# Performance work log

Measured on AMD Instinct MI355X. Metric: run time of the kernel, lower is better.

## Reference

```python
import jax, jax.numpy as jnp
import numpy as np

B, T, C, NH = 2, 2048, 1024, 16
HD = C // NH  # 64


def _ln(x, g, b, eps=1e-5):
    m = x.mean(-1, keepdims=True)
    v = ((x - m) ** 2).mean(-1, keepdims=True)
    return (x - m) / jnp.sqrt(v + eps) * g + b


def _ff(x, w1, b1, w2, b2):
    # Linear -> exact (erf) GELU -> Linear; dropout=0 (identity)
    return jax.nn.gelu(x @ w1 + b1, approximate=False) @ w2 + b2


def setup_inputs() -> dict:
    key = jax.random.key(0)
    ks = jax.random.split(key, 16)
    s = 0.02
    f32 = jnp.float32
    return {
        "x": jax.random.normal(ks[0], (B, T, C), f32),
        # SelfAttn qkv projection (torch Linear stored transposed: (in, out))
        "w_attn": jax.random.normal(ks[1], (C, 3 * C), f32) * s,
        "b_attn": jnp.zeros((3 * C,), f32),
        # SelfAttn's internal FeedForward
        "wa1": jax.random.normal(ks[2], (C, 4 * C), f32) * s,
        "ba1": jnp.zeros((4 * C,), f32),
        "wa2": jax.random.normal(ks[3], (4 * C, C), f32) * s,
        "ba2": jnp.zeros((C,), f32),
        # Block ln1
        "g1": jnp.ones((C,), f32),
        "be1": jnp.zeros((C,), f32),
        # Block FeedForward
        "wf1": jax.random.normal(ks[4], (C, 4 * C), f32) * s,
        "bf1": jnp.zeros((4 * C,), f32),
        "wf2": jax.random.normal(ks[5], (4 * C, C), f32) * s,
        "bf2": jnp.zeros((C,), f32),
        # Block ln2
        "g2": jnp.ones((C,), f32),
        "be2": jnp.zeros((C,), f32),
    }


def reference(x, w_attn, b_attn, wa1, ba1, wa2, ba2, g1, be1,
              wf1, bf1, wf2, bf2, g2, be2):
    Bx, Tx, Cx = x.shape
    qkv = x @ w_attn + b_attn  # (B, T, 3C)
    # NOTE: original splits as K, Q, V (in that order)
    K, Q, V = jnp.split(qkv, 3, axis=-1)

    def heads(t):  # (B, T, C) -> (B, NH, T, HD)
        return t.reshape(Bx, Tx, NH, HD).transpose(0, 2, 1, 3)

    Q, K, V = heads(Q), heads(K), heads(V)
    att = jnp.einsum('bhqd,bhkd->bhqk', Q, K) / np.float32(np.sqrt(HD))
    mask = jnp.tril(jnp.ones((Tx, Tx), bool))  # causal
    att = jnp.where(mask, att, -jnp.inf)
    att = jax.nn.softmax(att, axis=-1)
    y = jnp.einsum('bhqk,bhkd->bhqd', att, V)
    y = y.transpose(0, 2, 1, 3).reshape(Bx, Tx, Cx)
    # SelfAttn applies its own FeedForward (no output projection)
    y = _ff(y, wa1, ba1, wa2, ba2)
    # Block: post-sublayer LayerNorm, additive residuals
    x = x + _ln(y, g1, be1)
    x = x + _ln(_ff(x, wf1, bf1, wf2, bf2), g2, be2)
    return x
```

## Files before the change

kernel.cpp:

```cpp
#include <hip/hip_runtime.h>
#include <hip/hip_bf16.h>
#include <math.h>

#define Bz 2
#define Tz 2048
#define Cz 1024
#define NHz 16
#define HDz 64
#define Mz (Bz*Tz)

typedef unsigned short u16;
typedef __attribute__((ext_vector_type(8))) short bf16x8;
typedef __attribute__((ext_vector_type(4))) float f32x4;

__device__ __forceinline__ float bf2f(u16 u){
  union { unsigned int i; float f; } v; v.i = ((unsigned int)u) << 16; return v.f;
}
__device__ __forceinline__ u16 f2bf(float f){
  union { float f; unsigned int i; } v; v.f = f;
  return (u16)((v.i + 0x7fffu + ((v.i >> 16) & 1u)) >> 16);
}
__device__ __forceinline__ unsigned pack_bf_trunc(float a, float b){
  union { float f; unsigned u; } ua, ub; ua.f = a; ub.f = b;
  return (ua.u >> 16) | (ub.u & 0xffff0000u);
}
__device__ __forceinline__ float gelu_fast(float x){
  float x3 = x * x * x;
  float z2 = 1.5957691216057308f * (x + 0.044715f * x3);
  float e  = __expf(z2);
  float t  = 1.f - 2.f / (e + 1.f);
  return 0.5f * x * (1.f + t);
}

__device__ __forceinline__ void glds16(const void* g, void* l){
  __builtin_amdgcn_global_load_lds(
      (const __attribute__((address_space(1))) void*)g,
      (__attribute__((address_space(3))) void*)l, 16, 0, 0);
}

__global__ __launch_bounds__(256) void cast4_kernel(const float* __restrict__ in,
                                                    u16* __restrict__ out, int n4){
  int i = blockIdx.x * 256 + threadIdx.x;
  if (i < n4) {
    float4 v = ((const float4*)in)[i];
    u16 t[4] = { f2bf(v.x), f2bf(v.y), f2bf(v.z), f2bf(v.w) };
    *(uint2*)&out[(size_t)i * 4] = *(const uint2*)t;
  }
}

__global__ __launch_bounds__(256) void transpose5_kernel(
    const float* __restrict__ s0, const float* __restrict__ s1,
    const float* __restrict__ s2, const float* __restrict__ s3,
    const float* __restrict__ s4,
    u16* __restrict__ d0, u16* __restrict__ d1, u16* __restrict__ d2,
    u16* __restrict__ d3, u16* __restrict__ d4){
  __shared__ float tile[32][33];
  const int t = blockIdx.x;
  const float* src; u16* dst; int K, N, local;
  if (t < 3072)       { src = s0; dst = d0; K = 1024; N = 3072; local = t; }
  else if (t < 7168)  { src = s1; dst = d1; K = 1024; N = 4096; local = t - 3072; }
  else if (t < 11264) { src = s2; dst = d2; K = 4096; N = 1024; local = t - 7168; }
  else if (t < 15360) { src = s3; dst = d3; K = 1024; N = 4096; local = t - 11264; }
  else                { src = s4; dst = d4; K = 4096; N = 1024; local = t - 15360; }
  const int NT = N >> 5;
  const int kb = (local / NT) * 32, nb = (local % NT) * 32;
  const int tx = threadIdx.x & 31, ty = threadIdx.x >> 5;
  #pragma unroll
  for (int r = ty; r < 32; r += 8)
    tile[r][tx] = src[(size_t)(kb + r) * N + nb + tx];
  __syncthreads();
  #pragma unroll
  for (int r = ty; r < 32; r += 8)
    dst[(size_t)(nb + r) * K + kb + tx] = f2bf(tile[tx][r]);
}

template<int ACT>
__global__ __launch_bounds__(256) void gemm_kernel(const u16* __restrict__ A,
                                                   const u16* __restrict__ Bt,
                                                   const float* __restrict__ bias,
                                                   float* __restrict__ outf,
                                                   float* __restrict__ outf2,
                                                   u16* __restrict__ outb,
                                                   int N, int lda, int klen){
  __shared__ __align__(16) u16 As[2][128 * 32];
  __shared__ __align__(16) u16 Bs[2][128 * 32];
  const int tid  = threadIdx.x;
  const int wave = tid >> 6, lane = tid & 63;
  const int wm = (wave & 1) * 64, wn = (wave >> 1) * 64;
  const int m0 = blockIdx.x * 128, n0 = blockIdx.y * 128;
  const int kz = blockIdx.z;
  const int cc = lane & 15, quad = lane >> 4;
  const int lko = quad * 8;

  const u16* Ak  = A  + (size_t)kz * klen;
  const u16* Btk = Bt + (size_t)kz * klen;

  const int c = tid, c2 = tid + 256;
  const int row1 = c >> 2,  kc1 = (c & 3) * 8;
  const int row2 = c2 >> 2, kc2 = (c2 & 3) * 8;

  f32x4 acc[4][4] = {};

  const int nk = klen / 32;
  {
    glds16(Ak  + (size_t)(m0 + row1) * lda + kc1, &As[0][row1 * 32 + kc1]);
    glds16(Btk + (size_t)(n0 + row1) * lda + kc1, &Bs[0][row1 * 32 + kc1]);
    glds16(Ak  + (size_t)(m0 + row2) * lda + kc2, &As[0][row2 * 32 + kc2]);
    glds16(Btk + (size_t)(n0 + row2) * lda + kc2, &Bs[0][row2 * 32 + kc2]);
  }
  for (int ki = 0; ki < nk; ki++) {
    __syncthreads();
    if (ki + 1 < nk) {
      const int k0 = (ki + 1) * 32, bsel = (ki + 1) & 1;
      glds16(Ak  + (size_t)(m0 + row1) * lda + k0 + kc1, &As[bsel][row1 * 32 + kc1]);
      glds16(Btk + (size_t)(n0 + row1) * lda + k0 + kc1, &Bs[bsel][row1 * 32 + kc1]);
      glds16(Ak  + (size_t)(m0 + row2) * lda + k0 + kc2, &As[bsel][row2 * 32 + kc2]);
      glds16(Btk + (size_t)(n0 + row2) * lda + k0 + kc2, &Bs[bsel][row2 * 32 + kc2]);
    }
    const u16* Asb = As[ki & 1];
    const u16* Bsb = Bs[ki & 1];

    bf16x8 af[4], bfr[4];
    #pragma unroll
    for (int i = 0; i < 4; i++)
      af[i]  = *(const bf16x8*)&Asb[(wm + i * 16 + cc) * 32 + lko];
    #pragma unroll
    for (int j = 0; j < 4; j++)
      bfr[j] = *(const bf16x8*)&Bsb[(wn + j * 16 + cc) * 32 + lko];
    #pragma unroll
    for (int i = 0; i < 4; i++)
      #pragma unroll
      for (int j = 0; j < 4; j++)
        acc[i][j] = __builtin_amdgcn_mfma_f32_16x16x32_bf16(af[i], bfr[j], acc[i][j], 0, 0, 0);
  }

  const float* bias_k = (kz == 0) ? bias : nullptr;
  float* po = (kz == 0) ? outf : outf2;
  const int rbase = quad * 4;
  #pragma unroll
  for (int i = 0; i < 4; i++) {
    #pragma unroll
    for (int j = 0; j < 4; j++) {
      int col = n0 + wn + j * 16 + cc;
      float bv = bias_k ? bias_k[col] : 0.f;
      #pragma unroll
      for (int r = 0; r < 4; r++) {
        int row = m0 + wm + i * 16 + rbase + r;
        float v = acc[i][j][r] + bv;
        if (ACT == 1) v = gelu_fast(v);
        if (po)   po[(size_t)row * N + col]   = v;
        if (outb) outb[(size_t)row * N + col] = f2bf(v);
      }
    }
  }
}

__global__ __launch_bounds__(256) void vtrans_kernel(const u16* __restrict__ qkv,
                                                     u16* __restrict__ Vtb){
  __shared__ u16 Vl[64 * 72];
  const int tid = threadIdx.x;
  const int t0 = blockIdx.x * 64, h = blockIdx.y, b = blockIdx.z;
  const int bh = b * NHz + h;
  #pragma unroll
  for (int it = 0; it < 2; it++) {
    int c = tid + it * 256;
    int row = c >> 3, g = c & 7;
    *(uint4*)&Vl[row * 72 + g * 8] =
        *(const uint4*)(qkv + (size_t)(b * Tz + t0 + row) * (3 * Cz) + 2 * Cz + h * 64 + g * 8);
  }
  __syncthreads();
  #pragma unroll
  for (int it = 0; it < 2; it++) {
    int c = tid + it * 256;
    int d = c >> 3, tg = c & 7;
    u16 tmp[8];
    #pragma unroll
    for (int e = 0; e < 8; e++) tmp[e] = Vl[(tg * 8 + e) * 72 + d];
    *(uint4*)&Vtb[((size_t)bh * 64 + d) * Tz + t0 + tg * 8] = *(const uint4*)tmp;
  }
}

__global__ __launch_bounds__(256) void attn_kernel(const u16* __restrict__ qkv,
                                                   const u16* __restrict__ Vtb,
                                                   u16* __restrict__ y){
  __shared__ __align__(16) u16 KV[2][2][64 * 64];
  __shared__ __align__(16) u16 Ps[64 * 72];
  const int tid = threadIdx.x;
  const int lane = tid & 63, wave = tid >> 6;
  const int cc = lane & 15, quad = lane >> 4;
  const int h = blockIdx.y, b = blockIdx.z;
  const int bh = b * NHz + h;
  const size_t rowb = (size_t)b * Tz;
  const int wq0 = wave * 16;

  int foff[4][2];
  const int sw0 = (quad ^ (cc & 7)) * 8;
  const int sw1 = ((4 + quad) ^ (cc & 7)) * 8;
  #pragma unroll
  for (int t = 0; t < 4; ++t) {
    foff[t][0] = (t * 16 + cc) * 64 + sw0;
    foff[t][1] = (t * 16 + cc) * 64 + sw1;
  }
  const int pswb = (wq0 + cc) * 72 + quad * 4;
  const int psr0 = (wq0 + cc) * 72 + quad * 8;
  const int psr1 = (wq0 + cc) * 72 + 32 + quad * 8;

  auto stage = [&](int i, int bsel) {
    const int k0s = i * 64;
    #pragma unroll
    for (int it = 0; it < 2; ++it) {
      int ci = tid + it * 256;
      int row = ci >> 3, g = ci & 7;
      int gs = g ^ (row & 7);
      glds16(qkv + (rowb + k0s + row) * (3 * Cz) + h * 64 + gs * 8, &KV[bsel][0][ci * 8]);
      glds16(Vtb + ((size_t)bh * 64 + row) * Tz + k0s + gs * 8,     &KV[bsel][1][ci * 8]);
    }
  };

  for (int ph = 0; ph < 2; ++ph) {
    const int qt = ph ? (31 - (int)blockIdx.x) : (int)blockIdx.x;
    const int q0t = qt * 64 + wq0;
    const int nkt = qt + 1;
    const int wqmax = q0t + 15;

    bf16x8 qf[2];
    #pragma unroll
    for (int s = 0; s < 2; ++s)
      qf[s] = *(const bf16x8*)(qkv + (rowb + q0t + cc) * (3 * Cz)
                               + Cz + h * 64 + s * 32 + quad * 8);
    f32x4 acc[4] = {};
    float lp = 0.f;

    if (ph) __syncthreads();
    stage(0, 0);

    for (int i = 0; i < nkt; ++i) {
      __syncthreads();
      if (i + 1 < nkt) stage(i + 1, (i + 1) & 1);
      const int sel = i & 1;
      const u16* Kl = KV[sel][0];
      const u16* Vl = KV[sel][1];
      const int k0 = i * 64;
      if (k0 > wqmax) continue;

      bf16x8 kf[4][2];
      #pragma unroll
      for (int kt = 0; kt < 4; ++kt) {
        kf[kt][0] = *(const bf16x8*)&Kl[foff[kt][0]];
        kf[kt][1] = *(const bf16x8*)&Kl[foff[kt][1]];
      }
      const int qbase = q0t;
      #pragma unroll
      for (int kt = 0; kt < 4; ++kt) {
        const int kbase = k0 + kt * 16;
        uint2 pk;
        if (kbase > qbase + 15) {
          pk.x = 0u; pk.y = 0u;
        } else {
          f32x4 st = __builtin_amdgcn_mfma_f32_16x16x32_bf16(
              kf[kt][0], qf[0], (f32x4){0.f, 0.f, 0.f, 0.f}, 0, 0, 0);
          st = __builtin_amdgcn_mfma_f32_16x16x32_bf16(kf[kt][1], qf[1], st, 0, 0, 0);
          if (kbase + 15 > qbase) {
            const int kq = kbase + quad * 4, ql = qbase + cc;
            st[0] = (kq     <= ql) ? st[0] : -1e30f;
            st[1] = (kq + 1 <= ql) ? st[1] : -1e30f;
            st[2] = (kq + 2 <= ql) ? st[2] : -1e30f;
            st[3] = (kq + 3 <= ql) ? st[3] : -1e30f;
          }
          float p0 = __expf(fmaf(st[0], 0.125f, -16.f));
          float p1 = __expf(fmaf(st[1], 0.125f, -16.f));
          float p2 = __expf(fmaf(st[2], 0.125f, -16.f));
          float p3 = __expf(fmaf(st[3], 0.125f, -16.f));
          lp += (p0 + p1) + (p2 + p3);
          pk.x = pack_bf_trunc(p0, p1);
          pk.y = pack_bf_trunc(p2, p3);
        }
        *(uint2*)&Ps[pswb + kt * 16] = pk;
      }
      bf16x8 pf0 = *(const bf16x8*)&Ps[psr0];
      bf16x8 pf1 = *(const bf16x8*)&Ps[psr1];
      #pragma unroll
      for (int jd = 0; jd < 4; ++jd) {
        bf16x8 vf0 = *(const bf16x8*)&Vl[foff[jd][0]];
        bf16x8 vf1 = *(const bf16x8*)&Vl[foff[jd][1]];
        acc[jd] = __builtin_amdgcn_mfma_f32_16x16x32_bf16(pf0, vf0, acc[jd], 0, 0, 0);
        acc[jd] = __builtin_amdgcn_mfma_f32_16x16x32_bf16(pf1, vf1, acc[jd], 0, 0, 0);
      }
    }

    lp += __shfl_xor(lp, 16, 64);
    lp += __shfl_xor(lp, 32, 64);
    float inv[4];
    #pragma unroll
    for (int r = 0; r < 4; ++r) inv[r] = 1.f / __shfl(lp, quad * 4 + r, 64);
    #pragma unroll
    for (int jd = 0; jd < 4; ++jd)
      #pragma unroll
      for (int r = 0; r < 4; ++r) {
        int qrow = q0t + quad * 4 + r;
        y[(rowb + qrow) * Cz + h * 64 + jd * 16 + cc] = f2bf(acc[jd][r] * inv[r]);
      }
  }
}

__global__ __launch_bounds__(256) void ln_resid_kernel(const float* __restrict__ x,
                                                       const float* __restrict__ yin,
                                                       const float* __restrict__ yin2,
                                                       const float* __restrict__ g,
                                                       const float* __restrict__ be,
                                                       float* __restrict__ outf,
                                                       u16* __restrict__ outb){
  const int row = blockIdx.x;
  const int c0 = threadIdx.x * 4;
  const float* yr = yin + (size_t)row * Cz;
  const float* xr = x   + (size_t)row * Cz;
  float4 v = *(const float4*)(yr + c0);
  if (yin2) {
    float4 v2 = *(const float4*)(yin2 + (size_t)row * Cz + c0);
    v.x += v2.x; v.y += v2.y; v.z += v2.z; v.w += v2.w;
  }
  float s  = v.x + v.y + v.z + v.w;
  float s2 = v.x*v.x + v.y*v.y + v.z*v.z + v.w*v.w;
  #pragma unroll
  for (int off = 32; off > 0; off >>= 1) {
    s  += __shfl_down(s,  off);
    s2 += __shfl_down(s2, off);
  }
  __shared__ float ps[4], ps2[4];
  int wave = threadIdx.x >> 6, lane = threadIdx.x & 63;
  if (lane == 0) { ps[wave] = s; ps2[wave] = s2; }
  __syncthreads();
  s  = ps[0]  + ps[1]  + ps[2]  + ps[3];
  s2 = ps2[0] + ps2[1] + ps2[2] + ps2[3];
  const float mean = s * (1.f / Cz);
  const float var  = s2 * (1.f / Cz) - mean * mean;
  const float rstd = rsqrtf(var + 1e-5f);
  float4 xv = *(const float4*)(xr + c0);
  float4 gv = *(const float4*)(g + c0);
  float4 bv = *(const float4*)(be + c0);
  float4 ov;
  ov.x = xv.x + (v.x - mean) * rstd * gv.x + bv.x;
  ov.y = xv.y + (v.y - mean) * rstd * gv.y + bv.y;
  ov.z = xv.z + (v.z - mean) * rstd * gv.z + bv.z;
  ov.w = xv.w + (v.w - mean) * rstd * gv.w + bv.w;
  *(float4*)(outf + (size_t)row * Cz + c0) = ov;
  if (outb) {
    u16 t[4] = { f2bf(ov.x), f2bf(ov.y), f2bf(ov.z), f2bf(ov.w) };
    *(ulonglong1*)&outb[(size_t)row * Cz + c0] = *(const ulonglong1*)t;
  }
}

extern "C" void kernel_launch(void* const* d_in, const int* in_sizes, int n_in,
                              void* d_out, int out_size, void* d_ws, size_t ws_size,
                              hipStream_t stream) {
  const float* x      = (const float*)d_in[0];
  const float* w_attn = (const float*)d_in[1];
  const float* b_attn = (const float*)d_in[2];
  const float* wa1    = (const float*)d_in[3];
  const float* ba1    = (const float*)d_in[4];
  const float* wa2    = (const float*)d_in[5];
  const float* ba2    = (const float*)d_in[6];
  const float* g1     = (const float*)d_in[7];
  const float* be1    = (const float*)d_in[8];
  const float* wf1    = (const float*)d_in[9];
  const float* bf1    = (const float*)d_in[10];
  const float* wf2    = (const float*)d_in[11];
  const float* bf2    = (const float*)d_in[12];
  const float* g2     = (const float*)d_in[13];
  const float* be2    = (const float*)d_in[14];
  float* out = (float*)d_out;

  char* ws = (char*)d_ws;
  size_t off = 0;
  auto alloc = [&](size_t bytes) { size_t o = off; off += (bytes + 255) & ~(size_t)255; return o; };
  u16* xb      = (u16*)(ws + alloc((size_t)Mz * Cz * 2));
  u16* wT_attn = (u16*)(ws + alloc((size_t)3 * Cz * Cz * 2));
  u16* wT_a1   = (u16*)(ws + alloc((size_t)4 * Cz * Cz * 2));
  u16* wT_a2   = (u16*)(ws + alloc((size_t)4 * Cz * Cz * 2));
  u16* wT_f1   = (u16*)(ws + alloc((size_t)4 * Cz * Cz * 2));
  u16* wT_f2   = (u16*)(ws + alloc((size_t)4 * Cz * Cz * 2));
  u16* qkvb    = (u16*)(ws + alloc((size_t)Mz * 3 * Cz * 2));
  u16* Vtb     = (u16*)(ws + alloc((size_t)Bz * NHz * HDz * Tz * 2));
  u16* ybuf    = (u16*)(ws + alloc((size_t)Mz * Cz * 2));
  u16* hbuf    = (u16*)(ws + alloc((size_t)Mz * 4 * Cz * 2));
  float* vbuf  = (float*)(ws + alloc((size_t)Mz * Cz * 4));
  float* x1f   = (float*)(ws + alloc((size_t)Mz * Cz * 4));
  u16* x1b     = (u16*)(ws + alloc((size_t)Mz * Cz * 2));
  alloc(256);
  float* part1 = (float*)qkvb;
  (void)ws_size; (void)in_sizes; (void)n_in; (void)out_size;

  cast4_kernel<<<(Mz * Cz / 4 + 255) / 256, 256, 0, stream>>>(x, xb, Mz * Cz / 4);
  transpose5_kernel<<<19456, 256, 0, stream>>>(w_attn, wa1, wa2, wf1, wf2,
                                               wT_attn, wT_a1, wT_a2, wT_f1, wT_f2);

  gemm_kernel<0><<<dim3(Mz/128, 3*Cz/128, 1), 256, 0, stream>>>(xb, wT_attn, b_attn,
      nullptr, nullptr, qkvb, 3*Cz, Cz, Cz);

  vtrans_kernel<<<dim3(Tz/64, NHz, Bz), 256, 0, stream>>>(qkvb, Vtb);
  attn_kernel<<<dim3(16, NHz, Bz), 256, 0, stream>>>(qkvb, Vtb, ybuf);

  gemm_kernel<1><<<dim3(Mz/128, 4*Cz/128, 1), 256, 0, stream>>>(ybuf, wT_a1, ba1,
      nullptr, nullptr, hbuf, 4*Cz, Cz, Cz);
  gemm_kernel<0><<<dim3(Mz/128, Cz/128, 2), 256, 0, stream>>>(hbuf, wT_a2, ba2,
      vbuf, part1, nullptr, Cz, 4*Cz, 2*Cz);

  ln_resid_kernel<<<Mz, 256, 0, stream>>>(x, vbuf, part1, g1, be1, x1f, x1b);

  gemm_kernel<1><<<dim3(Mz/128, 4*Cz/128, 1), 256, 0, stream>>>(x1b, wT_f1, bf1,
      nullptr, nullptr, hbuf, 4*Cz, Cz, Cz);
  gemm_kernel<0><<<dim3(Mz/128, Cz/128, 2), 256, 0, stream>>>(hbuf, wT_f2, bf2,
      vbuf, part1, nullptr, Cz, 4*Cz, 2*Cz);

  ln_resid_kernel<<<Mz, 256, 0, stream>>>(x1f, vbuf, part1, g2, be2, out, nullptr);
}
```

Measured before the change: 505.4 us.

## Split-K down-projections four ways and drop GEMM LDS double buffering

Splits the K=4096 down-projection GEMMs into four K-slices instead of two, writing partial sums into scratch buffers that alias qkvb, ybuf and wT_attn. The LayerNorm-residual kernel now sums up to four partials. The GEMM main loop also drops LDS double buffering in favour of single-buffered load, sync, compute. This halves LDS per block, which may raise occupancy, but loads no longer overlap compute, and the extra partials add memory traffic.

After: 550.8 us. 9.0% more time.

```diff
diff --git a/kernel.cpp b/kernel.cpp
--- a/kernel.cpp
+++ b/kernel.cpp
@@ -78,12 +78,14 @@
 __global__ __launch_bounds__(256) void gemm_kernel(const u16* __restrict__ A,
                                                    const u16* __restrict__ Bt,
                                                    const float* __restrict__ bias,
-                                                   float* __restrict__ outf,
-                                                   float* __restrict__ outf2,
+                                                   float* __restrict__ po0,
+                                                   float* __restrict__ po1,
+                                                   float* __restrict__ po2,
+                                                   float* __restrict__ po3,
                                                    u16* __restrict__ outb,
                                                    int N, int lda, int klen){
-  __shared__ __align__(16) u16 As[2][128 * 32];
-  __shared__ __align__(16) u16 Bs[2][128 * 32];
+  __shared__ __align__(16) u16 As[128 * 32];
+  __shared__ __align__(16) u16 Bs[128 * 32];
   const int tid  = threadIdx.x;
   const int wave = tid >> 6, lane = tid & 63;
   const int wm = (wave & 1) * 64, wn = (wave >> 1) * 64;
@@ -95,38 +97,27 @@
   const u16* Ak  = A  + (size_t)kz * klen;
   const u16* Btk = Bt + (size_t)kz * klen;
 
-  const int c = tid, c2 = tid + 256;
-  const int row1 = c >> 2,  kc1 = (c & 3) * 8;
-  const int row2 = c2 >> 2, kc2 = (c2 & 3) * 8;
+  const int row1 = tid >> 2, kc1 = (tid & 3) * 8;
 
   f32x4 acc[4][4] = {};
 
   const int nk = klen / 32;
-  {
-    glds16(Ak  + (size_t)(m0 + row1) * lda + kc1, &As[0][row1 * 32 + kc1]);
-    glds16(Btk + (size_t)(n0 + row1) * lda + kc1, &Bs[0][row1 * 32 + kc1]);
-    glds16(Ak  + (size_t)(m0 + row2) * lda + kc2, &As[0][row2 * 32 + kc2]);
-    glds16(Btk + (size_t)(n0 + row2) * lda + kc2, &Bs[0][row2 * 32 + kc2]);
-  }
   for (int ki = 0; ki < nk; ki++) {
+    const int k0 = ki * 32;
     __syncthreads();
-    if (ki + 1 < nk) {
-      const int k0 = (ki + 1) * 32, bsel = (ki + 1) & 1;
-      glds16(Ak  + (size_t)(m0 + row1) * lda + k0 + kc1, &As[bsel][row1 * 32 + kc1]);
-      glds16(Btk + (size_t)(n0 + row1) * lda + k0 + kc1, &Bs[bsel][row1 * 32 + kc1]);
-      glds16(Ak  + (size_t)(m0 + row2) * lda + k0 + kc2, &As[bsel][row2 * 32 + kc2]);
-      glds16(Btk + (size_t)(n0 + row2) * lda + k0 + kc2, &Bs[bsel][row2 * 32 + kc2]);
-    }
-    const u16* Asb = As[ki & 1];
-    const u16* Bsb = Bs[ki & 1];
+    glds16(Ak  + (size_t)(m0 + row1) * lda + k0 + kc1,      &As[row1 * 32 + kc1]);
+    glds16(Btk + (size_t)(n0 + row1) * lda + k0 + kc1,      &Bs[row1 * 32 + kc1]);
+    glds16(Ak  + (size_t)(m0 + row1 + 64) * lda + k0 + kc1, &As[(row1 + 64) * 32 + kc1]);
+    glds16(Btk + (size_t)(n0 + row1 + 64) * lda + k0 + kc1, &Bs[(row1 + 64) * 32 + kc1]);
+    __syncthreads();
 
     bf16x8 af[4], bfr[4];
     #pragma unroll
     for (int i = 0; i < 4; i++)
-      af[i]  = *(const bf16x8*)&Asb[(wm + i * 16 + cc) * 32 + lko];
+      af[i]  = *(const bf16x8*)&As[(wm + i * 16 + cc) * 32 + lko];
     #pragma unroll
     for (int j = 0; j < 4; j++)
-      bfr[j] = *(const bf16x8*)&Bsb[(wn + j * 16 + cc) * 32 + lko];
+      bfr[j] = *(const bf16x8*)&Bs[(wn + j * 16 + cc) * 32 + lko];
     #pragma unroll
     for (int i = 0; i < 4; i++)
       #pragma unroll
@@ -135,7 +126,7 @@
   }
 
   const float* bias_k = (kz == 0) ? bias : nullptr;
-  float* po = (kz == 0) ? outf : outf2;
+  float* po = (kz == 0) ? po0 : (kz == 1) ? po1 : (kz == 2) ? po2 : po3;
   const int rbase = quad * 4;
   #pragma unroll
   for (int i = 0; i < 4; i++) {
@@ -304,21 +295,21 @@
 }
 
 __global__ __launch_bounds__(256) void ln_resid_kernel(const float* __restrict__ x,
-                                                       const float* __restrict__ yin,
-                                                       const float* __restrict__ yin2,
+                                                       const float* __restrict__ y1,
+                                                       const float* __restrict__ y2,
+                                                       const float* __restrict__ y3,
+                                                       const float* __restrict__ y4,
                                                        const float* __restrict__ g,
                                                        const float* __restrict__ be,
                                                        float* __restrict__ outf,
                                                        u16* __restrict__ outb){
   const int row = blockIdx.x;
   const int c0 = threadIdx.x * 4;
-  const float* yr = yin + (size_t)row * Cz;
-  const float* xr = x   + (size_t)row * Cz;
-  float4 v = *(const float4*)(yr + c0);
-  if (yin2) {
-    float4 v2 = *(const float4*)(yin2 + (size_t)row * Cz + c0);
-    v.x += v2.x; v.y += v2.y; v.z += v2.z; v.w += v2.w;
-  }
+  const size_t base = (size_t)row * Cz + c0;
+  float4 v = *(const float4*)(y1 + base);
+  if (y2) { float4 t = *(const float4*)(y2 + base); v.x+=t.x; v.y+=t.y; v.z+=t.z; v.w+=t.w; }
+  if (y3) { float4 t = *(const float4*)(y3 + base); v.x+=t.x; v.y+=t.y; v.z+=t.z; v.w+=t.w; }
+  if (y4) { float4 t = *(const float4*)(y4 + base); v.x+=t.x; v.y+=t.y; v.z+=t.z; v.w+=t.w; }
   float s  = v.x + v.y + v.z + v.w;
   float s2 = v.x*v.x + v.y*v.y + v.z*v.z + v.w*v.w;
   #pragma unroll
@@ -335,7 +326,7 @@
   const float mean = s * (1.f / Cz);
   const float var  = s2 * (1.f / Cz) - mean * mean;
   const float rstd = rsqrtf(var + 1e-5f);
-  float4 xv = *(const float4*)(xr + c0);
+  float4 xv = *(const float4*)(x + base);
   float4 gv = *(const float4*)(g + c0);
   float4 bv = *(const float4*)(be + c0);
   float4 ov;
@@ -343,10 +334,10 @@
   ov.y = xv.y + (v.y - mean) * rstd * gv.y + bv.y;
   ov.z = xv.z + (v.z - mean) * rstd * gv.z + bv.z;
   ov.w = xv.w + (v.w - mean) * rstd * gv.w + bv.w;
-  *(float4*)(outf + (size_t)row * Cz + c0) = ov;
+  *(float4*)(outf + base) = ov;
   if (outb) {
     u16 t[4] = { f2bf(ov.x), f2bf(ov.y), f2bf(ov.z), f2bf(ov.w) };
-    *(ulonglong1*)&outb[(size_t)row * Cz + c0] = *(const ulonglong1*)t;
+    *(ulonglong1*)&outb[base] = *(const ulonglong1*)t;
   }
 }
 
@@ -373,21 +364,23 @@
   char* ws = (char*)d_ws;
   size_t off = 0;
   auto alloc = [&](size_t bytes) { size_t o = off; off += (bytes + 255) & ~(size_t)255; return o; };
+  u16* qkvb    = (u16*)(ws + alloc((size_t)Mz * 3 * Cz * 2));
+  u16* ybuf    = (u16*)(ws + alloc((size_t)Mz * Cz * 2));
   u16* xb      = (u16*)(ws + alloc((size_t)Mz * Cz * 2));
   u16* wT_attn = (u16*)(ws + alloc((size_t)3 * Cz * Cz * 2));
   u16* wT_a1   = (u16*)(ws + alloc((size_t)4 * Cz * Cz * 2));
+  u16* Vtb     = (u16*)(ws + alloc((size_t)Bz * NHz * HDz * Tz * 2));
   u16* wT_a2   = (u16*)(ws + alloc((size_t)4 * Cz * Cz * 2));
   u16* wT_f1   = (u16*)(ws + alloc((size_t)4 * Cz * Cz * 2));
   u16* wT_f2   = (u16*)(ws + alloc((size_t)4 * Cz * Cz * 2));
-  u16* qkvb    = (u16*)(ws + alloc((size_t)Mz * 3 * Cz * 2));
-  u16* Vtb     = (u16*)(ws + alloc((size_t)Bz * NHz * HDz * Tz * 2));
-  u16* ybuf    = (u16*)(ws + alloc((size_t)Mz * Cz * 2));
   u16* hbuf    = (u16*)(ws + alloc((size_t)Mz * 4 * Cz * 2));
   float* vbuf  = (float*)(ws + alloc((size_t)Mz * Cz * 4));
   float* x1f   = (float*)(ws + alloc((size_t)Mz * Cz * 4));
   u16* x1b     = (u16*)(ws + alloc((size_t)Mz * Cz * 2));
   alloc(256);
   float* part1 = (float*)qkvb;
+  float* part2 = (float*)ybuf;
+  float* part3 = (float*)wT_attn;
   (void)ws_size; (void)in_sizes; (void)n_in; (void)out_size;
 
   cast4_kernel<<<(Mz * Cz / 4 + 255) / 256, 256, 0, stream>>>(x, xb, Mz * Cz / 4);
@@ -395,22 +388,24 @@
                                                wT_attn, wT_a1, wT_a2, wT_f1, wT_f2);
 
   gemm_kernel<0><<<dim3(Mz/128, 3*Cz/128, 1), 256, 0, stream>>>(xb, wT_attn, b_attn,
-      nullptr, nullptr, qkvb, 3*Cz, Cz, Cz);
+      nullptr, nullptr, nullptr, nullptr, qkvb, 3*Cz, Cz, Cz);
 
   vtrans_kernel<<<dim3(Tz/64, NHz, Bz), 256, 0, stream>>>(qkvb, Vtb);
   attn_kernel<<<dim3(16, NHz, Bz), 256, 0, stream>>>(qkvb, Vtb, ybuf);
 
   gemm_kernel<1><<<dim3(Mz/128, 4*Cz/128, 1), 256, 0, stream>>>(ybuf, wT_a1, ba1,
-      nullptr, nullptr, hbuf, 4*Cz, Cz, Cz);
-  gemm_kernel<0><<<dim3(Mz/128, Cz/128, 2), 256, 0, stream>>>(hbuf, wT_a2, ba2,
-      vbuf, part1, nullptr, Cz, 4*Cz, 2*Cz);
-
-  ln_resid_kernel<<<Mz, 256, 0, stream>>>(x, vbuf, part1, g1, be1, x1f, x1b);
+      nullptr, nullptr, nullptr, nullptr, hbuf, 4*Cz, Cz, Cz);
+  gemm_kernel<0><<<dim3(Mz/128, Cz/128, 4), 256, 0, stream>>>(hbuf, wT_a2, ba2,
+      vbuf, part1, part2, part3, nullptr, Cz, 4*Cz, Cz);
+
+  ln_resid_kernel<<<Mz, 256, 0, stream>>>(x, vbuf, part1, part2, part3,
+                                          g1, be1, x1f, x1b);
 
   gemm_kernel<1><<<dim3(Mz/128, 4*Cz/128, 1), 256, 0, stream>>>(x1b, wT_f1, bf1,
-      nullptr, nullptr, hbuf, 4*Cz, Cz, Cz);
-  gemm_kernel<0><<<dim3(Mz/128, Cz/128, 2), 256, 0, stream>>>(hbuf, wT_f2, bf2,
-      vbuf, part1, nullptr, Cz, 4*Cz, 2*Cz);
-
-  ln_resid_kernel<<<Mz, 256, 0, stream>>>(x1f, vbuf, part1, g2, be2, out, nullptr);
-}
+      nullptr, nullptr, nullptr, nullptr, hbuf, 4*Cz, Cz, Cz);
+  gemm_kernel<0><<<dim3(Mz/128, Cz/128, 4), 256, 0, stream>>>(hbuf, wT_f2, bf2,
+      vbuf, part1, part2, part3, nullptr, Cz, 4*Cz, Cz);
+
+  ln_resid_kernel<<<Mz, 256, 0, stream>>>(x1f, vbuf, part1, part2, part3,
+                                          g2, be2, out, nullptr);
+}
```
